# Kernel tuning notes

Measured on AMD Instinct MI355X. Metric: run time of the kernel, lower is better.

Reference implementation:

```python
import jax, jax.numpy as jnp
import numpy as np
import math

B, N, DQK, DV, M = 8, 8192, 128, 128, 256


def _make_omega(m: int, d: int, seed: int = 0) -> jnp.ndarray:
    """Block-orthogonal random feature matrix, shape [d, m] (matches torch _omega)."""
    rng = np.random.default_rng(seed)
    blocks = []
    nblocks = m // d
    for _ in range(nblocks):
        q, _ = np.linalg.qr(rng.standard_normal((d, d)))
        blocks.append(q.T)
    missing = m - nblocks * d
    if missing > 0:
        q, _ = np.linalg.qr(rng.standard_normal((d, d)))
        blocks.append(q.T[:missing])
    norm = np.linalg.norm(rng.standard_normal((m, d)), axis=1, keepdims=True)
    omega = (norm * np.vstack(blocks)).T  # [d, m]
    return jnp.asarray(omega, dtype=jnp.float32)


def setup_inputs() -> dict:
    key = jax.random.key(0)
    kq, kk, kv = jax.random.split(key, 3)
    Q = jax.random.normal(kq, (B, N, DQK), jnp.float32)
    K = jax.random.normal(kk, (B, N, DQK), jnp.float32)
    V = jax.random.normal(kv, (B, N, DV), jnp.float32)
    atom_mask = jnp.ones((B, N), jnp.float32)
    omega = _make_omega(M, DQK)
    return {"Q": Q, "K": K, "V": V, "atom_mask": atom_mask, "omega": omega}


def _phi(X, mask, omega, is_query: bool, eps: float = 1e-4):
    """Project into random-feature space with Performer stabilization."""
    d = X.shape[-1]
    m = omega.shape[-1]
    U = (X / d ** 0.25) @ omega                       # [B, N, m]
    h = jnp.sum(X * X, axis=-1, keepdims=True) / (2.0 * d ** 0.5)
    if is_query:
        mx = jnp.max(U, axis=-1, keepdims=True)       # per-token max
    else:
        mx = jnp.max(U, axis=(-2, -1), keepdims=True)  # per-batch max
    return (jnp.exp(U - h - mx) + eps) / math.sqrt(m) * mask[..., None]


def reference(Q, K, V, atom_mask, omega):
    eps = 1e-8
    Qp = _phi(Q, atom_mask, omega, True)   # [B, N, M]
    Kp = _phi(K, atom_mask, omega, False)  # [B, N, M]
    # norm_n = Qp_n . sum_j Kp_j
    norm = jnp.einsum('bnm,bm->bn', Qp, jnp.sum(Kp, axis=1))[..., None] + eps
    KV = jnp.einsum('bnm,bnv->bmv', Kp, V)             # [B, M, DV]
    return jnp.einsum('bnm,bmv->bnv', Qp, KV) / norm   # [B, N, DV]
```

## Files before the change

kernel.cpp:

```cpp
#include <hip/hip_runtime.h>
#include <math.h>

#define BB 8
#define NN 8192
#define DD 128
#define MM 256
#define DVV 128
#define PP 32
#define CHUNK 32

#define XSCALE 0.29730177875068026f
#define INV_SQRT_M 0.0625f

typedef _Float16 f16x8 __attribute__((ext_vector_type(8)));
typedef float f32x16 __attribute__((ext_vector_type(16)));

#define FR(s, l) ((s) * 520 + (l) * 8)

__device__ __forceinline__ unsigned f2ord(float f) {
    unsigned u = __float_as_uint(f);
    return (u & 0x80000000u) ? ~u : (u | 0x80000000u);
}
__device__ __forceinline__ float ord2f(unsigned u) {
    return (u & 0x80000000u) ? __uint_as_float(u & 0x7fffffffu) : __uint_as_float(~u);
}
__device__ __forceinline__ f32x16 mfma16(f16x8 a, f16x8 b, f32x16 c) {
    return __builtin_amdgcn_mfma_f32_32x32x16_f16(a, b, c, 0, 0, 0);
}
__device__ __forceinline__ int rowf(int r, int q) { return (r & 3) + 8 * (r >> 2) + 4 * q; }

__device__ __forceinline__ void stage_A(const float* __restrict__ src,
                                        _Float16* R1, float* hs, float* msk,
                                        const float* __restrict__ mrow, bool do_h) {
    const int tid = threadIdx.x;
    const int t = tid >> 3, ks = tid & 7;
    const float4* s4 = (const float4*)(src + t * DD + ks * 16);
    float x[16];
    #pragma unroll
    for (int u = 0; u < 4; ++u) {
        float4 v = s4[u];
        x[u*4+0] = v.x * XSCALE; x[u*4+1] = v.y * XSCALE;
        x[u*4+2] = v.z * XSCALE; x[u*4+3] = v.w * XSCALE;
    }
    if (do_h) {
        float p = 0.f;
        #pragma unroll
        for (int u = 0; u < 16; ++u) p += x[u] * x[u];
        p += __shfl_xor(p, 1, 64); p += __shfl_xor(p, 2, 64); p += __shfl_xor(p, 4, 64);
        if (ks == 0) { hs[t] = 0.5f * p; msk[t] = mrow[t]; }
    }
    #pragma unroll
    for (int q = 0; q < 2; ++q) {
        f16x8 h8, l8;
        #pragma unroll
        for (int j = 0; j < 8; ++j) {
            float xv = x[q*8 + j];
            _Float16 h = (_Float16)xv;
            h8[j] = h; l8[j] = (_Float16)(xv - (float)h);
        }
        *(f16x8*)&R1[FR(0*8 + ks, q*32 + t)] = h8;
        *(f16x8*)&R1[FR(1*8 + ks, q*32 + t)] = l8;
    }
}

__device__ __forceinline__ void stage_BV(const float* __restrict__ src, _Float16* R1) {
    const int tid = threadIdx.x;
    const int t = tid >> 3, c0 = (tid & 7) * 16;
    const int ts = t >> 4, qq = (t >> 3) & 1, j = t & 7;
    const float4* s4 = (const float4*)(src + t * DVV + c0);
    #pragma unroll
    for (int u = 0; u < 4; ++u) {
        float4 v = s4[u];
        float vv[4] = {v.x, v.y, v.z, v.w};
        #pragma unroll
        for (int e = 0; e < 4; ++e) {
            int c = c0 + u*4 + e;
            int vt = c >> 5, iv = c & 31;
            _Float16 h = (_Float16)vv[e];
            R1[FR((0*4 + vt)*2 + ts, qq*32 + iv) + j] = h;
            R1[FR((1*4 + vt)*2 + ts, qq*32 + iv) + j] = (_Float16)(vv[e] - (float)h);
        }
    }
}

__global__ __launch_bounds__(256) void pack_kernel(const float* __restrict__ omega,
                                                   _Float16* __restrict__ omh,
                                                   _Float16* __restrict__ oml,
                                                   unsigned* __restrict__ kmaxord) {
    int g = blockIdx.x * 256 + threadIdx.x;
    if (g < BB) kmaxord[g] = f2ord(-INFINITY);
    int lane = g & 63, ks = (g >> 6) & 7, nt = g >> 9;
    int q = lane >> 5, i = lane & 31;
    f16x8 h8, l8;
    #pragma unroll
    for (int j = 0; j < 8; ++j) {
        float w = omega[(size_t)(ks*16 + q*8 + j) * MM + nt*32 + i];
        _Float16 h = (_Float16)w;
        h8[j] = h; l8[j] = (_Float16)(w - (float)h);
    }
    ((f16x8*)omh)[g] = h8;
    ((f16x8*)oml)[g] = l8;
}

__global__ __launch_bounds__(256, 2) void kmax_kernel(const float* __restrict__ K,
                                                      const _Float16* __restrict__ omh,
                                                      unsigned* __restrict__ kmaxord) {
    __shared__ __align__(16) _Float16 R1[16 * 520];
    __shared__ float wred[4];
    const int b = blockIdx.y;
    const int tid = threadIdx.x, w = tid >> 6, lane = tid & 63;

    f16x8 om[2][8];
    #pragma unroll
    for (int n = 0; n < 2; ++n)
        #pragma unroll
        for (int k = 0; k < 8; ++k)
            om[n][k] = ((const f16x8*)omh)[((2*w + n)*8 + k)*64 + lane];

    float mx = -INFINITY;
    for (int c = 0; c < 8; ++c) {
        int t0 = (blockIdx.x * 8 + c) * CHUNK;
        __syncthreads();
        stage_A(K + ((size_t)b*NN + t0) * DD, R1, nullptr, nullptr, nullptr, false);
        __syncthreads();
        f32x16 a0, a1;
        #pragma unroll
        for (int r = 0; r < 16; ++r) { a0[r] = 0.f; a1[r] = 0.f; }
        #pragma unroll
        for (int ks = 0; ks < 8; ++ks) {
            f16x8 ah = *(const f16x8*)&R1[FR(ks, lane)];
            a0 = mfma16(ah, om[0][ks], a0);
            a1 = mfma16(ah, om[1][ks], a1);
        }
        #pragma unroll
        for (int r = 0; r < 16; ++r) mx = fmaxf(mx, fmaxf(a0[r], a1[r]));
    }
    #pragma unroll
    for (int off = 1; off < 64; off <<= 1) mx = fmaxf(mx, __shfl_xor(mx, off, 64));
    if (lane == 0) wred[w] = mx;
    __syncthreads();
    if (tid == 0)
        atomicMax(kmaxord + b,
                  f2ord(fmaxf(fmaxf(wred[0], wred[1]), fmaxf(wred[2], wred[3]))));
}

__global__ __launch_bounds__(256) void kv_kernel(const float* __restrict__ K,
                                                 const float* __restrict__ V,
                                                 const float* __restrict__ mask,
                                                 const _Float16* __restrict__ omh,
                                                 const _Float16* __restrict__ oml,
                                                 const unsigned* __restrict__ kmaxord,
                                                 float* __restrict__ pkv,
                                                 float* __restrict__ pks) {
    __shared__ __align__(16) _Float16 R1[16 * 520];
    __shared__ __align__(16) _Float16 R2[32 * 520];
    __shared__ float hs[32], msk[32];
    const int b = blockIdx.y, p = blockIdx.x;
    const int tid = threadIdx.x, w = tid >> 6, lane = tid & 63;
    const int i = tid & 31, q = (tid >> 5) & 1;
    const float kmaxv = ord2f(kmaxord[b]);

    f16x8 omf[2][2][8];
    #pragma unroll
    for (int n = 0; n < 2; ++n)
        #pragma unroll
        for (int k = 0; k < 8; ++k) {
            omf[0][n][k] = ((const f16x8*)omh)[((2*w + n)*8 + k)*64 + lane];
            omf[1][n][k] = ((const f16x8*)oml)[((2*w + n)*8 + k)*64 + lane];
        }

    f32x16 kvacc[2][4];
    #pragma unroll
    for (int f = 0; f < 2; ++f)
        #pragma unroll
        for (int vt = 0; vt < 4; ++vt)
            #pragma unroll
            for (int r = 0; r < 16; ++r) kvacc[f][vt][r] = 0.f;
    float ksa[2] = {0.f, 0.f};

    for (int c = 0; c < 8; ++c) {
        int t0 = (p * 8 + c) * CHUNK;
        __syncthreads();
        stage_A(K + ((size_t)b*NN + t0) * DD, R1, hs, msk,
                mask + (size_t)b*NN + t0, true);
        __syncthreads();

        f32x16 a0, a1;
        #pragma unroll
        for (int r = 0; r < 16; ++r) { a0[r] = 0.f; a1[r] = 0.f; }
        #pragma unroll
        for (int ks = 0; ks < 8; ++ks) {
            f16x8 ah = *(const f16x8*)&R1[FR(ks, lane)];
            f16x8 al = *(const f16x8*)&R1[FR(8 + ks, lane)];
            a0 = mfma16(ah, omf[0][0][ks], a0);
            a0 = mfma16(ah, omf[1][0][ks], a0);
            a0 = mfma16(al, omf[0][0][ks], a0);
            a1 = mfma16(ah, omf[0][1][ks], a1);
            a1 = mfma16(ah, omf[1][1][ks], a1);
            a1 = mfma16(al, omf[0][1][ks], a1);
        }
        __syncthreads();

        stage_BV(V + ((size_t)b*NN + t0) * DVV, R1);
        #pragma unroll
        for (int r = 0; r < 16; ++r) {
            int tok = rowf(r, q);
            float hh = hs[tok] + kmaxv;
            float mm = msk[tok] * INV_SQRT_M;
            int ts = tok >> 4, qq = (tok >> 3) & 1, j = tok & 7;
            {
                float kp = (__expf(a0[r] - hh) + 1e-4f) * mm;
                ksa[0] += kp;
                _Float16 h = (_Float16)kp;
                R2[FR((2*w + 0)*2 + ts, qq*32 + i) + j] = h;
                R2[FR(16 + (2*w + 0)*2 + ts, qq*32 + i) + j] = (_Float16)(kp - (float)h);
            }
            {
                float kp = (__expf(a1[r] - hh) + 1e-4f) * mm;
                ksa[1] += kp;
                _Float16 h = (_Float16)kp;
                R2[FR((2*w + 1)*2 + ts, qq*32 + i) + j] = h;
                R2[FR(16 + (2*w + 1)*2 + ts, qq*32 + i) + j] = (_Float16)(kp - (float)h);
            }
        }
        __syncthreads();

        #pragma unroll
        for (int f = 0; f < 2; ++f) {
            int ft = 2*w + f;
            f16x8 ah[2], al[2];
            #pragma unroll
            for (int ts = 0; ts < 2; ++ts) {
                ah[ts] = *(const f16x8*)&R2[FR(ft*2 + ts, lane)];
                al[ts] = *(const f16x8*)&R2[FR(16 + ft*2 + ts, lane)];
            }
            #pragma unroll
            for (int vt = 0; vt < 4; ++vt) {
                #pragma unroll
                for (int ts = 0; ts < 2; ++ts) {
                    f16x8 bh = *(const f16x8*)&R1[FR(vt*2 + ts, lane)];
                    f16x8 bl = *(const f16x8*)&R1[FR(8 + vt*2 + ts, lane)];
                    kvacc[f][vt] = mfma16(ah[ts], bh, kvacc[f][vt]);
                    kvacc[f][vt] = mfma16(ah[ts], bl, kvacc[f][vt]);
                    kvacc[f][vt] = mfma16(al[ts], bh, kvacc[f][vt]);
                }
            }
        }
    }

    float* dst = pkv + ((size_t)(b * PP + p) << 15);
    #pragma unroll
    for (int f = 0; f < 2; ++f)
        #pragma unroll
        for (int vt = 0; vt < 4; ++vt)
            #pragma unroll
            for (int r = 0; r < 16; ++r) {
                int feat = (2*w + f)*32 + rowf(r, q);
                dst[feat * DVV + vt*32 + i] = kvacc[f][vt][r];
            }
    #pragma unroll
    for (int n = 0; n < 2; ++n) {
        float s = ksa[n] + __shfl_xor(ksa[n], 32, 64);
        if (q == 0) pks[(size_t)(b * PP + p) * MM + (2*w + n)*32 + i] = s;
    }
}

__global__ __launch_bounds__(256) void reduce_kernel(const float* __restrict__ pkv,
                                                     const float* __restrict__ pks,
                                                     float* __restrict__ ksum,
                                                     _Float16* __restrict__ kvph,
                                                     _Float16* __restrict__ kvpl) {
    const int b = blockIdx.y;
    int g = blockIdx.x * 256 + threadIdx.x;
    float s = 0.f;
    for (int p = 0; p < PP; ++p) s += pkv[((size_t)(b * PP + p) << 15) + g];
    int f = g >> 7, v = g & 127;
    int vt = v >> 5, iv = v & 31, fs = f >> 4, qq = (f >> 3) & 1, j = f & 7;
    size_t idx = (size_t)b * 32768 + (size_t)((vt*16 + fs)*64 + qq*32 + iv)*8 + j;
    _Float16 h = (_Float16)s;
    kvph[idx] = h;
    kvpl[idx] = (_Float16)(s - (float)h);
    if (blockIdx.x == 0) {
        float ss = 0.f;
        for (int p = 0; p < PP; ++p) ss += pks[(size_t)(b * PP + p) * MM + g];
        ksum[b * MM + g] = ss;
    }
}

__global__ __launch_bounds__(256) void out_kernel(const float* __restrict__ Q,
                                                  const float* __restrict__ mask,
                                                  const _Float16* __restrict__ omh,
                                                  const _Float16* __restrict__ oml,
                                                  const float* __restrict__ ksum,
                                                  const _Float16* __restrict__ kvph,
                                                  const _Float16* __restrict__ kvpl,
                                                  float* __restrict__ out) {
    __shared__ __align__(16) _Float16 R1[16 * 520];
    __shared__ __align__(16) _Float16 R2[32 * 520];
    __shared__ float hs[32], msk[32], wmax[4][32], norms[32];
    const int b = blockIdx.y;
    const int tid = threadIdx.x, w = tid >> 6, lane = tid & 63;
    const int i = tid & 31, q = (tid >> 5) & 1;

    f16x8 omf[2][2][8];
    #pragma unroll
    for (int n = 0; n < 2; ++n)
        #pragma unroll
        for (int k = 0; k < 8; ++k) {
            omf[0][n][k] = ((const f16x8*)omh)[((2*w + n)*8 + k)*64 + lane];
            omf[1][n][k] = ((const f16x8*)oml)[((2*w + n)*8 + k)*64 + lane];
        }
    f16x8 bfh[16], bfl[16];
    #pragma unroll
    for (int fs = 0; fs < 16; ++fs) {
        bfh[fs] = ((const f16x8*)kvph)[(size_t)b * 4096 + (w*16 + fs)*64 + lane];
        bfl[fs] = ((const f16x8*)kvpl)[(size_t)b * 4096 + (w*16 + fs)*64 + lane];
    }
    f16x8 bnh[4], bnl[4];
    #pragma unroll
    for (int u = 0; u < 4; ++u) {
        f16x8 hh, ll;
        #pragma unroll
        for (int j = 0; j < 8; ++j) { hh[j] = (_Float16)0.f; ll[j] = (_Float16)0.f; }
        if (i == 0) {
            #pragma unroll
            for (int j = 0; j < 8; ++j) {
                float s = ksum[b * MM + (4*w + u)*16 + q*8 + j];
                _Float16 h = (_Float16)s;
                hh[j] = h; ll[j] = (_Float16)(s - (float)h);
            }
        }
        bnh[u] = hh; bnl[u] = ll;
    }

    for (int c = 0; c < 8; ++c) {
        int t0 = (blockIdx.x * 8 + c) * CHUNK;
        __syncthreads();
        stage_A(Q + ((size_t)b*NN + t0) * DD, R1, hs, msk,
                mask + (size_t)b*NN + t0, true);
        if (tid < 32) norms[tid] = 1e-8f;
        __syncthreads();

        f32x16 a0, a1;
        #pragma unroll
        for (int r = 0; r < 16; ++r) { a0[r] = 0.f; a1[r] = 0.f; }
        #pragma unroll
        for (int ks = 0; ks < 8; ++ks) {
            f16x8 ah = *(const f16x8*)&R1[FR(ks, lane)];
            f16x8 al = *(const f16x8*)&R1[FR(8 + ks, lane)];
            a0 = mfma16(ah, omf[0][0][ks], a0);
            a0 = mfma16(ah, omf[1][0][ks], a0);
            a0 = mfma16(al, omf[0][0][ks], a0);
            a1 = mfma16(ah, omf[0][1][ks], a1);
            a1 = mfma16(ah, omf[1][1][ks], a1);
            a1 = mfma16(al, omf[0][1][ks], a1);
        }
        float tm[16];
        #pragma unroll
        for (int r = 0; r < 16; ++r) tm[r] = fmaxf(a0[r], a1[r]);
        #pragma unroll
        for (int off = 1; off < 32; off <<= 1)
            #pragma unroll
            for (int r = 0; r < 16; ++r) tm[r] = fmaxf(tm[r], __shfl_xor(tm[r], off, 64));
        if (i == 0)
            #pragma unroll
            for (int r = 0; r < 16; ++r) wmax[w][rowf(r, q)] = tm[r];
        __syncthreads();

        #pragma unroll
        for (int r = 0; r < 16; ++r) {
            int tok = rowf(r, q);
            float tmax = fmaxf(fmaxf(wmax[0][tok], wmax[1][tok]),
                               fmaxf(wmax[2][tok], wmax[3][tok]));
            float hh = hs[tok] + tmax;
            float mm = msk[tok] * INV_SQRT_M;
            #pragma unroll
            for (int n = 0; n < 2; ++n) {
                float qp = (__expf((n ? a1[r] : a0[r]) - hh) + 1e-4f) * mm;
                int feat = (2*w + n)*32 + i;
                int fstep = feat >> 4, fq = (i >> 3) & 1, fj = i & 7;
                _Float16 h = (_Float16)qp;
                R2[FR(fstep, fq*32 + tok) + fj] = h;
                R2[FR(16 + fstep, fq*32 + tok) + fj] = (_Float16)(qp - (float)h);
            }
        }
        __syncthreads();

        f32x16 oa, na;
        #pragma unroll
        for (int r = 0; r < 16; ++r) { oa[r] = 0.f; na[r] = 0.f; }
        #pragma unroll
        for (int fs = 0; fs < 16; ++fs) {
            f16x8 ah = *(const f16x8*)&R2[FR(fs, lane)];
            f16x8 al = *(const f16x8*)&R2[FR(16 + fs, lane)];
            oa = mfma16(ah, bfh[fs], oa);
            oa = mfma16(ah, bfl[fs], oa);
            oa = mfma16(al, bfh[fs], oa);
        }
        #pragma unroll
        for (int u = 0; u < 4; ++u) {
            f16x8 ah = *(const f16x8*)&R2[FR(4*w + u, lane)];
            f16x8 al = *(const f16x8*)&R2[FR(16 + 4*w + u, lane)];
            na = mfma16(ah, bnh[u], na);
            na = mfma16(ah, bnl[u], na);
            na = mfma16(al, bnh[u], na);
        }
        if (i == 0)
            #pragma unroll
            for (int r = 0; r < 16; ++r) atomicAdd(&norms[rowf(r, q)], na[r]);
        __syncthreads();

        float* ob = out + ((size_t)b*NN + t0) * DVV + w*32 + i;
        #pragma unroll
        for (int r = 0; r < 16; ++r) {
            int tok = rowf(r, q);
            ob[(size_t)tok * DVV] = oa[r] / norms[tok];
        }
    }
}

extern "C" void kernel_launch(void* const* d_in, const int* in_sizes, int n_in,
                              void* d_out, int out_size, void* d_ws, size_t ws_size,
                              hipStream_t stream) {
    const float* Q     = (const float*)d_in[0];
    const float* K     = (const float*)d_in[1];
    const float* V     = (const float*)d_in[2];
    const float* mask  = (const float*)d_in[3];
    const float* omega = (const float*)d_in[4];
    float* out = (float*)d_out;

    char* ws = (char*)d_ws;
    _Float16* omh    = (_Float16*)(ws);
    _Float16* oml    = (_Float16*)(ws + (64 << 10));
    unsigned* kmaxord = (unsigned*)(ws + (128 << 10));
    float*    ksum   = (float*)(ws + (132 << 10));
    float*    pks    = (float*)(ws + (140 << 10));
    _Float16* kvph   = (_Float16*)(ws + (400 << 10));
    _Float16* kvpl   = (_Float16*)(ws + (912 << 10));
    float*    pkv    = (float*)(ws + (2 << 20));

    pack_kernel<<<16, 256, 0, stream>>>(omega, omh, oml, kmaxord);
    kmax_kernel<<<dim3(32, BB), 256, 0, stream>>>(K, omh, kmaxord);
    kv_kernel<<<dim3(PP, BB), 256, 0, stream>>>(K, V, mask, omh, oml, kmaxord, pkv, pks);
    reduce_kernel<<<dim3(128, BB), 256, 0, stream>>>(pkv, pks, ksum, kvph, kvpl);
    out_kernel<<<dim3(32, BB), 256, 0, stream>>>(Q, mask, omh, oml, ksum, kvph, kvpl, out);
}
```

Before: 248.2 us.

## Double grid sizes: split kv features across blocks, halve chunks per block

The kv kernel now splits the 256 random features into two halves handled by separate blocks, so each wave owns one 32-feature tile and register and LDS use drop. That allows two blocks per CU. The kmax and out kernels process half as many chunks per block with twice as many blocks, which fills more CUs. Division by the norm is replaced with a hardware reciprocal. The cost is that each kv block recomputes the K staging and V loads for its half of the features, doubling K/V global reads, and the reciprocal is slightly less exact than true division.

New measurement: 315.3 us. +27.0%, slower.

```diff
diff --git a/kernel.cpp b/kernel.cpp
--- a/kernel.cpp
+++ b/kernel.cpp
@@ -118,8 +118,8 @@
             om[n][k] = ((const f16x8*)omh)[((2*w + n)*8 + k)*64 + lane];
 
     float mx = -INFINITY;
-    for (int c = 0; c < 8; ++c) {
-        int t0 = (blockIdx.x * 8 + c) * CHUNK;
+    for (int c = 0; c < 4; ++c) {
+        int t0 = (blockIdx.x * 4 + c) * CHUNK;
         __syncthreads();
         stage_A(K + ((size_t)b*NN + t0) * DD, R1, nullptr, nullptr, nullptr, false);
         __syncthreads();
@@ -144,39 +144,39 @@
                   f2ord(fmaxf(fmaxf(wred[0], wred[1]), fmaxf(wred[2], wred[3]))));
 }
 
-__global__ __launch_bounds__(256) void kv_kernel(const float* __restrict__ K,
-                                                 const float* __restrict__ V,
-                                                 const float* __restrict__ mask,
-                                                 const _Float16* __restrict__ omh,
-                                                 const _Float16* __restrict__ oml,
-                                                 const unsigned* __restrict__ kmaxord,
-                                                 float* __restrict__ pkv,
-                                                 float* __restrict__ pks) {
+__global__ __launch_bounds__(256, 2) void kv_kernel(const float* __restrict__ K,
+                                                    const float* __restrict__ V,
+                                                    const float* __restrict__ mask,
+                                                    const _Float16* __restrict__ omh,
+                                                    const _Float16* __restrict__ oml,
+                                                    const unsigned* __restrict__ kmaxord,
+                                                    float* __restrict__ pkv,
+                                                    float* __restrict__ pks) {
     __shared__ __align__(16) _Float16 R1[16 * 520];
-    __shared__ __align__(16) _Float16 R2[32 * 520];
+    __shared__ __align__(16) _Float16 R2[16 * 520];
     __shared__ float hs[32], msk[32];
-    const int b = blockIdx.y, p = blockIdx.x;
+    const int b = blockIdx.y, bx = blockIdx.x;
+    const int rest = bx >> 3;
+    const int h = rest & 1;
+    const int p = (rest >> 1) * 8 + (bx & 7);
     const int tid = threadIdx.x, w = tid >> 6, lane = tid & 63;
     const int i = tid & 31, q = (tid >> 5) & 1;
+    const int nt = h * 4 + w;
     const float kmaxv = ord2f(kmaxord[b]);
 
-    f16x8 omf[2][2][8];
-    #pragma unroll
-    for (int n = 0; n < 2; ++n)
-        #pragma unroll
-        for (int k = 0; k < 8; ++k) {
-            omf[0][n][k] = ((const f16x8*)omh)[((2*w + n)*8 + k)*64 + lane];
-            omf[1][n][k] = ((const f16x8*)oml)[((2*w + n)*8 + k)*64 + lane];
-        }
-
-    f32x16 kvacc[2][4];
-    #pragma unroll
-    for (int f = 0; f < 2; ++f)
-        #pragma unroll
-        for (int vt = 0; vt < 4; ++vt)
-            #pragma unroll
-            for (int r = 0; r < 16; ++r) kvacc[f][vt][r] = 0.f;
-    float ksa[2] = {0.f, 0.f};
+    f16x8 omf[2][8];
+    #pragma unroll
+    for (int k = 0; k < 8; ++k) {
+        omf[0][k] = ((const f16x8*)omh)[(nt*8 + k)*64 + lane];
+        omf[1][k] = ((const f16x8*)oml)[(nt*8 + k)*64 + lane];
+    }
+
+    f32x16 kvacc[4];
+    #pragma unroll
+    for (int vt = 0; vt < 4; ++vt)
+        #pragma unroll
+        for (int r = 0; r < 16; ++r) kvacc[vt][r] = 0.f;
+    float ksa = 0.f;
 
     for (int c = 0; c < 8; ++c) {
         int t0 = (p * 8 + c) * CHUNK;
@@ -185,19 +185,16 @@
                 mask + (size_t)b*NN + t0, true);
         __syncthreads();
 
-        f32x16 a0, a1;
-        #pragma unroll
-        for (int r = 0; r < 16; ++r) { a0[r] = 0.f; a1[r] = 0.f; }
+        f32x16 a0;
+        #pragma unroll
+        for (int r = 0; r < 16; ++r) a0[r] = 0.f;
         #pragma unroll
         for (int ks = 0; ks < 8; ++ks) {
             f16x8 ah = *(const f16x8*)&R1[FR(ks, lane)];
             f16x8 al = *(const f16x8*)&R1[FR(8 + ks, lane)];
-            a0 = mfma16(ah, omf[0][0][ks], a0);
-            a0 = mfma16(ah, omf[1][0][ks], a0);
-            a0 = mfma16(al, omf[0][0][ks], a0);
-            a1 = mfma16(ah, omf[0][1][ks], a1);
-            a1 = mfma16(ah, omf[1][1][ks], a1);
-            a1 = mfma16(al, omf[0][1][ks], a1);
+            a0 = mfma16(ah, omf[0][ks], a0);
+            a0 = mfma16(ah, omf[1][ks], a0);
+            a0 = mfma16(al, omf[0][ks], a0);
         }
         __syncthreads();
 
@@ -207,61 +204,45 @@
             int tok = rowf(r, q);
             float hh = hs[tok] + kmaxv;
             float mm = msk[tok] * INV_SQRT_M;
+            float kp = (__expf(a0[r] - hh) + 1e-4f) * mm;
+            ksa += kp;
             int ts = tok >> 4, qq = (tok >> 3) & 1, j = tok & 7;
-            {
-                float kp = (__expf(a0[r] - hh) + 1e-4f) * mm;
-                ksa[0] += kp;
-                _Float16 h = (_Float16)kp;
-                R2[FR((2*w + 0)*2 + ts, qq*32 + i) + j] = h;
-                R2[FR(16 + (2*w + 0)*2 + ts, qq*32 + i) + j] = (_Float16)(kp - (float)h);
+            _Float16 hv = (_Float16)kp;
+            R2[FR(w*2 + ts, qq*32 + i) + j] = hv;
+            R2[FR(8 + w*2 + ts, qq*32 + i) + j] = (_Float16)(kp - (float)hv);
+        }
+        __syncthreads();
+
+        f16x8 ah2[2], al2[2];
+        #pragma unroll
+        for (int ts = 0; ts < 2; ++ts) {
+            ah2[ts] = *(const f16x8*)&R2[FR(w*2 + ts, lane)];
+            al2[ts] = *(const f16x8*)&R2[FR(8 + w*2 + ts, lane)];
+        }
+        #pragma unroll
+        for (int vt = 0; vt < 4; ++vt) {
+            #pragma unroll
+            for (int ts = 0; ts < 2; ++ts) {
+                f16x8 bh = *(const f16x8*)&R1[FR(vt*2 + ts, lane)];
+                f16x8 bl = *(const f16x8*)&R1[FR(8 + vt*2 + ts, lane)];
+                kvacc[vt] = mfma16(ah2[ts], bh, kvacc[vt]);
+                kvacc[vt] = mfma16(ah2[ts], bl, kvacc[vt]);
+                kvacc[vt] = mfma16(al2[ts], bh, kvacc[vt]);
             }
-            {
-                float kp = (__expf(a1[r] - hh) + 1e-4f) * mm;
-                ksa[1] += kp;
-                _Float16 h = (_Float16)kp;
-                R2[FR((2*w + 1)*2 + ts, qq*32 + i) + j] = h;
-                R2[FR(16 + (2*w + 1)*2 + ts, qq*32 + i) + j] = (_Float16)(kp - (float)h);
-            }
-        }
-        __syncthreads();
-
-        #pragma unroll
-        for (int f = 0; f < 2; ++f) {
-            int ft = 2*w + f;
-            f16x8 ah[2], al[2];
-            #pragma unroll
-            for (int ts = 0; ts < 2; ++ts) {
-                ah[ts] = *(const f16x8*)&R2[FR(ft*2 + ts, lane)];
-                al[ts] = *(const f16x8*)&R2[FR(16 + ft*2 + ts, lane)];
-            }
-            #pragma unroll
-            for (int vt = 0; vt < 4; ++vt) {
-                #pragma unroll
-                for (int ts = 0; ts < 2; ++ts) {
-                    f16x8 bh = *(const f16x8*)&R1[FR(vt*2 + ts, lane)];
-                    f16x8 bl = *(const f16x8*)&R1[FR(8 + vt*2 + ts, lane)];
-                    kvacc[f][vt] = mfma16(ah[ts], bh, kvacc[f][vt]);
-                    kvacc[f][vt] = mfma16(ah[ts], bl, kvacc[f][vt]);
-                    kvacc[f][vt] = mfma16(al[ts], bh, kvacc[f][vt]);
-                }
-            }
         }
     }
 
     float* dst = pkv + ((size_t)(b * PP + p) << 15);
     #pragma unroll
-    for (int f = 0; f < 2; ++f)
-        #pragma unroll
-        for (int vt = 0; vt < 4; ++vt)
-            #pragma unroll
-            for (int r = 0; r < 16; ++r) {
-                int feat = (2*w + f)*32 + rowf(r, q);
-                dst[feat * DVV + vt*32 + i] = kvacc[f][vt][r];
-            }
-    #pragma unroll
-    for (int n = 0; n < 2; ++n) {
-        float s = ksa[n] + __shfl_xor(ksa[n], 32, 64);
-        if (q == 0) pks[(size_t)(b * PP + p) * MM + (2*w + n)*32 + i] = s;
+    for (int vt = 0; vt < 4; ++vt)
+        #pragma unroll
+        for (int r = 0; r < 16; ++r) {
+            int feat = nt*32 + rowf(r, q);
+            dst[feat * DVV + vt*32 + i] = kvacc[vt][r];
+        }
+    {
+        float s = ksa + __shfl_xor(ksa, 32, 64);
+        if (q == 0) pks[(size_t)(b * PP + p) * MM + nt*32 + i] = s;
     }
 }
 
@@ -287,14 +268,14 @@
     }
 }
 
-__global__ __launch_bounds__(256) void out_kernel(const float* __restrict__ Q,
-                                                  const float* __restrict__ mask,
-                                                  const _Float16* __restrict__ omh,
-                                                  const _Float16* __restrict__ oml,
-                                                  const float* __restrict__ ksum,
-                                                  const _Float16* __restrict__ kvph,
-                                                  const _Float16* __restrict__ kvpl,
-                                                  float* __restrict__ out) {
+__global__ __launch_bounds__(256, 2) void out_kernel(const float* __restrict__ Q,
+                                                     const float* __restrict__ mask,
+                                                     const _Float16* __restrict__ omh,
+                                                     const _Float16* __restrict__ oml,
+                                                     const float* __restrict__ ksum,
+                                                     const _Float16* __restrict__ kvph,
+                                                     const _Float16* __restrict__ kvpl,
+                                                     float* __restrict__ out) {
     __shared__ __align__(16) _Float16 R1[16 * 520];
     __shared__ __align__(16) _Float16 R2[32 * 520];
     __shared__ float hs[32], msk[32], wmax[4][32], norms[32];
@@ -333,8 +314,8 @@
         bnh[u] = hh; bnl[u] = ll;
     }
 
-    for (int c = 0; c < 8; ++c) {
-        int t0 = (blockIdx.x * 8 + c) * CHUNK;
+    for (int c = 0; c < 4; ++c) {
+        int t0 = (blockIdx.x * 4 + c) * CHUNK;
         __syncthreads();
         stage_A(Q + ((size_t)b*NN + t0) * DD, R1, hs, msk,
                 mask + (size_t)b*NN + t0, true);
@@ -414,7 +395,7 @@
         #pragma unroll
         for (int r = 0; r < 16; ++r) {
             int tok = rowf(r, q);
-            ob[(size_t)tok * DVV] = oa[r] / norms[tok];
+            ob[(size_t)tok * DVV] = oa[r] * __builtin_amdgcn_rcpf(norms[tok]);
         }
     }
 }
@@ -440,8 +421,8 @@
     float*    pkv    = (float*)(ws + (2 << 20));
 
     pack_kernel<<<16, 256, 0, stream>>>(omega, omh, oml, kmaxord);
-    kmax_kernel<<<dim3(32, BB), 256, 0, stream>>>(K, omh, kmaxord);
-    kv_kernel<<<dim3(PP, BB), 256, 0, stream>>>(K, V, mask, omh, oml, kmaxord, pkv, pks);
+    kmax_kernel<<<dim3(64, BB), 256, 0, stream>>>(K, omh, kmaxord);
+    kv_kernel<<<dim3(64, BB), 256, 0, stream>>>(K, V, mask, omh, oml, kmaxord, pkv, pks);
     reduce_kernel<<<dim3(128, BB), 256, 0, stream>>>(pkv, pks, ksum, kvph, kvpl);
-    out_kernel<<<dim3(32, BB), 256, 0, stream>>>(Q, mask, omh, oml, ksum, kvph, kvpl, out);
-}
+    out_kernel<<<dim3(64, BB), 256, 0, stream>>>(Q, mask, omh, oml, ksum, kvph, kvpl, out);
+}
```
